# Performance work log

Measured on AMD Instinct MI355X. Metric: run time of the kernel, lower is better.

## Reference

```python
import jax, jax.numpy as jnp
import numpy as np

N_NODES = 100000
N_EDGES = 1600000
IN_DIM = 128
OUT_DIM = 32
LEAKY_SLOPE = 0.2  # tf.nn.leaky_relu default alpha
NEG_INF = -1e30


def setup_inputs() -> dict:
    key = jax.random.key(0)
    k1, k2, k3, k4, k5, k6 = jax.random.split(key, 6)
    node_embeddings = jax.random.normal(k1, (N_NODES, IN_DIM), dtype=jnp.float32)
    # glorot-uniform-like scaling for params
    W_n = jax.random.normal(k2, (IN_DIM, OUT_DIM), dtype=jnp.float32) * (1.0 / np.sqrt(IN_DIM))
    a_src = jax.random.normal(k3, (OUT_DIM,), dtype=jnp.float32) * (1.0 / np.sqrt(OUT_DIM))
    a_dst = jax.random.normal(k4, (OUT_DIM,), dtype=jnp.float32) * (1.0 / np.sqrt(OUT_DIM))
    src = jax.random.randint(k5, (N_EDGES,), 0, N_NODES, dtype=jnp.int32)
    dst = jnp.sort(jax.random.randint(k6, (N_EDGES,), 0, N_NODES, dtype=jnp.int32))
    return {"node_embeddings": node_embeddings, "W_n": W_n, "a_src": a_src,
            "a_dst": a_dst, "src": src, "dst": dst}


def reference(node_embeddings, W_n, a_src, a_dst, src, dst):
    # Linear transform: [n, d]
    z = node_embeddings @ W_n
    # Per-node attention scalars (z @ a_src / z @ a_dst), then gather per edge.
    s_src = z @ a_src  # [n]
    s_dst = z @ a_dst  # [n]
    e = jax.nn.leaky_relu(s_src[src] + s_dst[dst], negative_slope=LEAKY_SLOPE)  # [E]
    # Segment softmax over incoming edges of each dst node.
    e_max = jax.ops.segment_max(e, dst, num_segments=N_NODES, indices_are_sorted=True)
    e_max = jnp.where(jnp.isfinite(e_max), e_max, 0.0)  # zero-degree nodes
    e_exp = jnp.exp(e - e_max[dst])
    denom = jax.ops.segment_sum(e_exp, dst, num_segments=N_NODES, indices_are_sorted=True)
    alpha = e_exp / jnp.where(denom > 0, denom, 1.0)[dst]  # [E]
    # Weighted aggregation of src-transformed features onto dst.
    agg = jax.ops.segment_sum(alpha[:, None] * z[src], dst,
                              num_segments=N_NODES, indices_are_sorted=True)
    return jax.nn.relu(agg)  # [n, d]
```

## Files before the change

kernel.cpp:

```cpp
#include <hip/hip_runtime.h>
#include <math.h>

#define N_NODES 100000
#define N_EDGES 1600000
#define IN_DIM  128
#define OUT_DIM 32
#define LEAKY   0.2f

typedef unsigned int uint;
typedef unsigned short ushort;
typedef __attribute__((ext_vector_type(8))) short bf16x8;
typedef __attribute__((ext_vector_type(4))) float f32x4;

__device__ __forceinline__ ushort rne16(float f) {
    uint u = __float_as_uint(f);
    return (ushort)((u + 0x7fffu + ((u >> 16) & 1u)) >> 16);
}

__global__ __launch_bounds__(256) void gemm_s_kernel(
    const float* __restrict__ X, const float* __restrict__ W,
    const float* __restrict__ a_src, const float* __restrict__ a_dst,
    ushort* __restrict__ zu16, float* __restrict__ ssrc, float* __restrict__ sdst)
{
    const int lane = threadIdx.x & 63;
    const int wv   = threadIdx.x >> 6;
    const int m    = lane & 15;
    const int kg   = lane >> 4;

    const int rowA = blockIdx.x * 64 + wv * 16 + m;
    const int rA   = (rowA < N_NODES) ? rowA : (N_NODES - 1);
    const float* xp = X + (size_t)rA * IN_DIM + (kg << 3);

    float4 xA[4], xB[4];
    #pragma unroll
    for (int s = 0; s < 4; ++s) {
        xA[s] = *reinterpret_cast<const float4*>(xp + (s << 5));
        xB[s] = *reinterpret_cast<const float4*>(xp + (s << 5) + 4);
    }

    bf16x8 b0[4], b1[4];
    #pragma unroll
    for (int s = 0; s < 4; ++s) {
        #pragma unroll
        for (int j = 0; j < 8; ++j) {
            const int k = (s << 5) + (kg << 3) + j;
            b0[s][j] = (short)rne16(W[k * OUT_DIM + m]);
            b1[s][j] = (short)rne16(W[k * OUT_DIM + m + 16]);
        }
    }

    f32x4 acc0 = {0.f, 0.f, 0.f, 0.f};
    f32x4 acc1 = {0.f, 0.f, 0.f, 0.f};

    #pragma unroll
    for (int s = 0; s < 4; ++s) {
        float xs[8] = {xA[s].x, xA[s].y, xA[s].z, xA[s].w,
                       xB[s].x, xB[s].y, xB[s].z, xB[s].w};
        bf16x8 ah, al;
        #pragma unroll
        for (int j = 0; j < 8; ++j) {
            const uint u = __float_as_uint(xs[j]);
            ah[j] = (short)(u >> 16);
            const float lo = xs[j] - __uint_as_float(u & 0xffff0000u);
            al[j] = (short)(__float_as_uint(lo) >> 16);
        }
        acc0 = __builtin_amdgcn_mfma_f32_16x16x32_bf16(ah, b0[s], acc0, 0, 0, 0);
        acc0 = __builtin_amdgcn_mfma_f32_16x16x32_bf16(al, b0[s], acc0, 0, 0, 0);
        acc1 = __builtin_amdgcn_mfma_f32_16x16x32_bf16(ah, b1[s], acc1, 0, 0, 0);
        acc1 = __builtin_amdgcn_mfma_f32_16x16x32_bf16(al, b1[s], acc1, 0, 0, 0);
    }

    const float as0 = a_src[m], as1 = a_src[m + 16];
    const float ad0 = a_dst[m], ad1 = a_dst[m + 16];
    float ps[4], pd[4];
    #pragma unroll
    for (int r = 0; r < 4; ++r) {
        ps[r] = acc0[r] * as0 + acc1[r] * as1;
        pd[r] = acc0[r] * ad0 + acc1[r] * ad1;
    }
    #pragma unroll
    for (int r = 0; r < 4; ++r) {
        #pragma unroll
        for (int msk = 1; msk <= 8; msk <<= 1) {
            ps[r] += __shfl_xor(ps[r], msk, 64);
            pd[r] += __shfl_xor(pd[r], msk, 64);
        }
    }

    const int rbase = blockIdx.x * 64 + wv * 16 + (kg << 2);
    if (m == 0) {
        #pragma unroll
        for (int r = 0; r < 4; ++r)
            if (rbase + r < N_NODES) ssrc[rbase + r] = ps[r];
    }
    if (m == 1) {
        #pragma unroll
        for (int r = 0; r < 4; ++r)
            if (rbase + r < N_NODES) sdst[rbase + r] = pd[r];
    }

    #pragma unroll
    for (int r = 0; r < 4; ++r) {
        const int row = rbase + r;
        if (row < N_NODES) {
            zu16[row * OUT_DIM + m]      = rne16(acc0[r]);
            zu16[row * OUT_DIM + m + 16] = rne16(acc1[r]);
        }
    }
}

__global__ __launch_bounds__(256) void edge_prep_kernel(
    const int* __restrict__ dst, const int* __restrict__ src,
    const float* __restrict__ ssrc, const float* __restrict__ sdst,
    int* __restrict__ off, float* __restrict__ wgt)
{
    const int e = blockIdx.x * blockDim.x + threadIdx.x;
    if (e >= N_EDGES) return;
    const int d = dst[e];
    const int dprev = (e == 0) ? -1 : dst[e - 1];
    for (int n = dprev + 1; n <= d; ++n) off[n] = e;
    if (e == N_EDGES - 1) {
        for (int n = d + 1; n <= N_NODES; ++n) off[n] = N_EDGES;
    }
    float x = ssrc[src[e]] + sdst[d];
    x = (x > 0.f) ? x : LEAKY * x;
    wgt[e] = __expf(x);
}

__global__ __launch_bounds__(256) void agg_kernel(
    const uint* __restrict__ zu, const float* __restrict__ wgt,
    const int* __restrict__ src, const int* __restrict__ off,
    float* __restrict__ out)
{
    __shared__ float2 sw[8][40];
    const int t = threadIdx.x;
    const int g = t >> 5, c = t & 31;
    const int n = blockIdx.x * 8 + g;
    if (n >= N_NODES) return;

    const int lo = off[n], hi = off[n + 1];
    const int eh = c >> 4, ci = c & 15;

    float ax = 0.f, ay = 0.f, den = 0.f;

    for (int base = lo; base < hi; base += 32) {
        const int cnt = min(32, hi - base);
        if (c < 8) sw[g][cnt + c] = make_float2(0.f, __int_as_float(0));
        if (c < cnt) {
            const int e = base + c;
            const float wv = wgt[e];
            const int s16 = src[e] << 4;
            den += wv;
            sw[g][c] = make_float2(wv, __int_as_float(s16));
        }
        int nsteps = (cnt + 1) >> 1;
        nsteps = (nsteps + 3) & ~3;
        for (int j0 = 0; j0 < nsteps; j0 += 4) {
            const float2 p0 = sw[g][2 * (j0 + 0) + eh];
            const float2 p1 = sw[g][2 * (j0 + 1) + eh];
            const float2 p2 = sw[g][2 * (j0 + 2) + eh];
            const float2 p3 = sw[g][2 * (j0 + 3) + eh];
            const uint u0 = zu[__float_as_int(p0.y) + ci];
            const uint u1 = zu[__float_as_int(p1.y) + ci];
            const uint u2 = zu[__float_as_int(p2.y) + ci];
            const uint u3 = zu[__float_as_int(p3.y) + ci];
            ax = fmaf(p0.x, __uint_as_float(u0 << 16), ax);
            ay = fmaf(p0.x, __uint_as_float(u0 & 0xffff0000u), ay);
            ax = fmaf(p1.x, __uint_as_float(u1 << 16), ax);
            ay = fmaf(p1.x, __uint_as_float(u1 & 0xffff0000u), ay);
            ax = fmaf(p2.x, __uint_as_float(u2 << 16), ax);
            ay = fmaf(p2.x, __uint_as_float(u2 & 0xffff0000u), ay);
            ax = fmaf(p3.x, __uint_as_float(u3 << 16), ax);
            ay = fmaf(p3.x, __uint_as_float(u3 & 0xffff0000u), ay);
        }
    }

    ax += __shfl_xor(ax, 16, 64);
    ay += __shfl_xor(ay, 16, 64);
    #pragma unroll
    for (int msk = 16; msk >= 1; msk >>= 1) den += __shfl_xor(den, msk, 64);

    if (eh == 0) {
        const float inv = (den > 0.f) ? (1.f / den) : 0.f;
        float2 o;
        o.x = fmaxf(ax * inv, 0.f);
        o.y = fmaxf(ay * inv, 0.f);
        *reinterpret_cast<float2*>(&out[n * OUT_DIM + (ci << 1)]) = o;
    }
}

extern "C" void kernel_launch(void* const* d_in, const int* in_sizes, int n_in,
                              void* d_out, int out_size, void* d_ws, size_t ws_size,
                              hipStream_t stream) {
    const float* X     = (const float*)d_in[0];
    const float* W     = (const float*)d_in[1];
    const float* a_src = (const float*)d_in[2];
    const float* a_dst = (const float*)d_in[3];
    const int*   src   = (const int*)d_in[4];
    const int*   dst   = (const int*)d_in[5];
    float* out = (float*)d_out;

    char* ws = (char*)d_ws;
    ushort* zu16 = (ushort*)ws; ws += (size_t)N_NODES * OUT_DIM * sizeof(ushort);
    float* ssrc  = (float*)ws;  ws += (size_t)N_NODES * sizeof(float);
    float* sdst  = (float*)ws;  ws += (size_t)N_NODES * sizeof(float);
    int*   off   = (int*)ws;    ws += (size_t)(N_NODES + 1) * sizeof(int);
    float* wgt   = (float*)ws;  ws += (size_t)N_EDGES * sizeof(float);

    gemm_s_kernel<<<(N_NODES + 63) / 64, 256, 0, stream>>>(X, W, a_src, a_dst, zu16, ssrc, sdst);
    edge_prep_kernel<<<(N_EDGES + 255) / 256, 256, 0, stream>>>(dst, src, ssrc, sdst, off, wgt);
    agg_kernel<<<(N_NODES + 7) / 8, 256, 0, stream>>>((const uint*)zu16, wgt, src, off, out);
}
```

Baseline: 52.09 us.

## Fuse edge attention weight computation into aggregation and widen feature gathers

Edge score computation (leaky relu and exp of gathered node scalars) moves out of the separate edge kernel and into the aggregation kernel, so the per-edge weight array is no longer written and read back from global memory. The offsets computation becomes its own light kernel launched before the GEMM. The aggregation now uses 8 edges in parallel with 4 lanes each loading 16-byte chunks of a bf16 row instead of 2 edges with 16 lanes loading 4 bytes, which cuts the number of gather instructions. The cost is more accumulator registers and a wider cross-lane reduction.

```diff
diff --git a/kernel.cpp b/kernel.cpp
--- a/kernel.cpp
+++ b/kernel.cpp
@@ -109,10 +109,8 @@
     }
 }
 
-__global__ __launch_bounds__(256) void edge_prep_kernel(
-    const int* __restrict__ dst, const int* __restrict__ src,
-    const float* __restrict__ ssrc, const float* __restrict__ sdst,
-    int* __restrict__ off, float* __restrict__ wgt)
+__global__ __launch_bounds__(256) void offsets_kernel(
+    const int* __restrict__ dst, int* __restrict__ off)
 {
     const int e = blockIdx.x * blockDim.x + threadIdx.x;
     if (e >= N_EDGES) return;
@@ -122,70 +120,81 @@
     if (e == N_EDGES - 1) {
         for (int n = d + 1; n <= N_NODES; ++n) off[n] = N_EDGES;
     }
-    float x = ssrc[src[e]] + sdst[d];
-    x = (x > 0.f) ? x : LEAKY * x;
-    wgt[e] = __expf(x);
 }
 
 __global__ __launch_bounds__(256) void agg_kernel(
-    const uint* __restrict__ zu, const float* __restrict__ wgt,
-    const int* __restrict__ src, const int* __restrict__ off,
-    float* __restrict__ out)
+    const uint* __restrict__ zu, const float* __restrict__ ssrc,
+    const float* __restrict__ sdst, const int* __restrict__ src,
+    const int* __restrict__ off, float* __restrict__ out)
 {
-    __shared__ float2 sw[8][40];
+    __shared__ float2 sw[8][64];
     const int t = threadIdx.x;
     const int g = t >> 5, c = t & 31;
     const int n = blockIdx.x * 8 + g;
     if (n >= N_NODES) return;
 
     const int lo = off[n], hi = off[n + 1];
-    const int eh = c >> 4, ci = c & 15;
-
-    float ax = 0.f, ay = 0.f, den = 0.f;
+    const float sd = sdst[n];
+    const int eh = c >> 2;
+    const int ci = c & 3;
+
+    float a0 = 0.f, a1 = 0.f, a2 = 0.f, a3 = 0.f;
+    float a4 = 0.f, a5 = 0.f, a6 = 0.f, a7 = 0.f;
+    float den = 0.f;
 
     for (int base = lo; base < hi; base += 32) {
         const int cnt = min(32, hi - base);
-        if (c < 8) sw[g][cnt + c] = make_float2(0.f, __int_as_float(0));
+        sw[g][cnt + c] = make_float2(0.f, __int_as_float(0));
         if (c < cnt) {
             const int e = base + c;
-            const float wv = wgt[e];
-            const int s16 = src[e] << 4;
-            den += wv;
-            sw[g][c] = make_float2(wv, __int_as_float(s16));
-        }
-        int nsteps = (cnt + 1) >> 1;
-        nsteps = (nsteps + 3) & ~3;
-        for (int j0 = 0; j0 < nsteps; j0 += 4) {
-            const float2 p0 = sw[g][2 * (j0 + 0) + eh];
-            const float2 p1 = sw[g][2 * (j0 + 1) + eh];
-            const float2 p2 = sw[g][2 * (j0 + 2) + eh];
-            const float2 p3 = sw[g][2 * (j0 + 3) + eh];
-            const uint u0 = zu[__float_as_int(p0.y) + ci];
-            const uint u1 = zu[__float_as_int(p1.y) + ci];
-            const uint u2 = zu[__float_as_int(p2.y) + ci];
-            const uint u3 = zu[__float_as_int(p3.y) + ci];
-            ax = fmaf(p0.x, __uint_as_float(u0 << 16), ax);
-            ay = fmaf(p0.x, __uint_as_float(u0 & 0xffff0000u), ay);
-            ax = fmaf(p1.x, __uint_as_float(u1 << 16), ax);
-            ay = fmaf(p1.x, __uint_as_float(u1 & 0xffff0000u), ay);
-            ax = fmaf(p2.x, __uint_as_float(u2 << 16), ax);
-            ay = fmaf(p2.x, __uint_as_float(u2 & 0xffff0000u), ay);
-            ax = fmaf(p3.x, __uint_as_float(u3 << 16), ax);
-            ay = fmaf(p3.x, __uint_as_float(u3 & 0xffff0000u), ay);
-        }
-    }
-
-    ax += __shfl_xor(ax, 16, 64);
-    ay += __shfl_xor(ay, 16, 64);
+            const int s = src[e];
+            float x = ssrc[s] + sd;
+            x = (x > 0.f) ? x : LEAKY * x;
+            const float v = __expf(x);
+            den += v;
+            sw[g][c] = make_float2(v, __int_as_float(s << 4));
+        }
+        const float2 p0 = sw[g][eh];
+        const float2 p1 = sw[g][8 + eh];
+        const float2 p2 = sw[g][16 + eh];
+        const float2 p3 = sw[g][24 + eh];
+        const uint4 u0 = *reinterpret_cast<const uint4*>(zu + __float_as_int(p0.y) + (ci << 2));
+        const uint4 u1 = *reinterpret_cast<const uint4*>(zu + __float_as_int(p1.y) + (ci << 2));
+        const uint4 u2 = *reinterpret_cast<const uint4*>(zu + __float_as_int(p2.y) + (ci << 2));
+        const uint4 u3 = *reinterpret_cast<const uint4*>(zu + __float_as_int(p3.y) + (ci << 2));
+        #define ACC8(P, U)                                                  \
+            a0 = fmaf(P.x, __uint_as_float(U.x << 16),         a0);         \
+            a1 = fmaf(P.x, __uint_as_float(U.x & 0xffff0000u), a1);         \
+            a2 = fmaf(P.x, __uint_as_float(U.y << 16),         a2);         \
+            a3 = fmaf(P.x, __uint_as_float(U.y & 0xffff0000u), a3);         \
+            a4 = fmaf(P.x, __uint_as_float(U.z << 16),         a4);         \
+            a5 = fmaf(P.x, __uint_as_float(U.z & 0xffff0000u), a5);         \
+            a6 = fmaf(P.x, __uint_as_float(U.w << 16),         a6);         \
+            a7 = fmaf(P.x, __uint_as_float(U.w & 0xffff0000u), a7);
+        ACC8(p0, u0) ACC8(p1, u1) ACC8(p2, u2) ACC8(p3, u3)
+        #undef ACC8
+    }
+
+    #pragma unroll
+    for (int msk = 4; msk <= 16; msk <<= 1) {
+        a0 += __shfl_xor(a0, msk, 64); a1 += __shfl_xor(a1, msk, 64);
+        a2 += __shfl_xor(a2, msk, 64); a3 += __shfl_xor(a3, msk, 64);
+        a4 += __shfl_xor(a4, msk, 64); a5 += __shfl_xor(a5, msk, 64);
+        a6 += __shfl_xor(a6, msk, 64); a7 += __shfl_xor(a7, msk, 64);
+    }
     #pragma unroll
     for (int msk = 16; msk >= 1; msk >>= 1) den += __shfl_xor(den, msk, 64);
 
     if (eh == 0) {
         const float inv = (den > 0.f) ? (1.f / den) : 0.f;
-        float2 o;
-        o.x = fmaxf(ax * inv, 0.f);
-        o.y = fmaxf(ay * inv, 0.f);
-        *reinterpret_cast<float2*>(&out[n * OUT_DIM + (ci << 1)]) = o;
+        float4 o0, o1;
+        o0.x = fmaxf(a0 * inv, 0.f); o0.y = fmaxf(a1 * inv, 0.f);
+        o0.z = fmaxf(a2 * inv, 0.f); o0.w = fmaxf(a3 * inv, 0.f);
+        o1.x = fmaxf(a4 * inv, 0.f); o1.y = fmaxf(a5 * inv, 0.f);
+        o1.z = fmaxf(a6 * inv, 0.f); o1.w = fmaxf(a7 * inv, 0.f);
+        float* op = &out[n * OUT_DIM + (ci << 3)];
+        *reinterpret_cast<float4*>(op)     = o0;
+        *reinterpret_cast<float4*>(op + 4) = o1;
     }
 }
 
@@ -205,9 +214,8 @@
     float* ssrc  = (float*)ws;  ws += (size_t)N_NODES * sizeof(float);
     float* sdst  = (float*)ws;  ws += (size_t)N_NODES * sizeof(float);
     int*   off   = (int*)ws;    ws += (size_t)(N_NODES + 1) * sizeof(int);
-    float* wgt   = (float*)ws;  ws += (size_t)N_EDGES * sizeof(float);
-
+
+    offsets_kernel<<<(N_EDGES + 255) / 256, 256, 0, stream>>>(dst, off);
     gemm_s_kernel<<<(N_NODES + 63) / 64, 256, 0, stream>>>(X, W, a_src, a_dst, zu16, ssrc, sdst);
-    edge_prep_kernel<<<(N_EDGES + 255) / 256, 256, 0, stream>>>(dst, src, ssrc, sdst, off, wgt);
-    agg_kernel<<<(N_NODES + 7) / 8, 256, 0, stream>>>((const uint*)zu16, wgt, src, off, out);
-}
+    agg_kernel<<<(N_NODES + 7) / 8, 256, 0, stream>>>((const uint*)zu16, ssrc, sdst, src, off, out);
+}
```

Result: faster. 49.39 us (-5.2%).
